# Kernel optimization log

Hardware: AMD Instinct MI355X
Metric: run time of the kernel (lower is better)

## Reference

```python
import jax, jax.numpy as jnp
import numpy as np

B, C, H, W, O = 8, 128, 256, 256, 128


def setup_inputs() -> dict:
    key = jax.random.key(0)
    k1, k2, k3, k4 = jax.random.split(key, 4)
    x = jax.random.normal(k1, (B, C, H, W), dtype=jnp.float32)
    theta_s = jax.random.uniform(k2, (C, 2), dtype=jnp.float32, minval=-1.0, maxval=1.0)
    w_dw = jax.random.normal(k3, (C,), dtype=jnp.float32) * 0.1   # depthwise 1x1, groups=C
    w_pw = jax.random.normal(k4, (O, C), dtype=jnp.float32) * (1.0 / np.sqrt(C))  # pointwise 1x1
    return {"x": x, "theta_s": theta_s, "w_dw": w_dw, "w_pw": w_pw}


def reference(x, theta_s, w_dw, w_pw):
    b, c, h, w = x.shape
    # zero pad by 1 (ZeroPad2d(1)); shift operates on the padded map, output is interior
    xp = jnp.pad(x, ((0, 0), (0, 0), (1, 1), (1, 1)))
    hp, wp = h + 2, w + 2
    t = -theta_s                      # (C, 2); torch code negates theta
    ft = jnp.floor(t)
    dt = t - ft                       # fractional part, (C, 2)
    ft = ft.astype(jnp.int32)
    # interior grid of the padded map: rows/cols 1..h / 1..w
    m = jnp.arange(1, h + 1)
    n = jnp.arange(1, w + 1)
    y0 = jnp.clip(m[None, :] + ft[:, 0:1], 0, hp - 1)      # (C, h)
    y1 = jnp.clip(m[None, :] + ft[:, 0:1] + 1, 0, hp - 1)  # (C, h)
    x0 = jnp.clip(n[None, :] + ft[:, 1:2], 0, wp - 1)      # (C, w)
    x1 = jnp.clip(n[None, :] + ft[:, 1:2] + 1, 0, wp - 1)  # (C, w)
    cidx = jnp.arange(c)[:, None, None]                    # (C,1,1)
    # gather four bilinear corners for all channels at once -> (B, C, h, w)
    z1 = xp[:, cidx, y0[:, :, None], x0[:, None, :]]
    z2 = xp[:, cidx, y0[:, :, None], x1[:, None, :]]
    z3 = xp[:, cidx, y1[:, :, None], x0[:, None, :]]
    z4 = xp[:, cidx, y1[:, :, None], x1[:, None, :]]
    dy = dt[:, 0][None, :, None, None]
    dx = dt[:, 1][None, :, None, None]
    s = (z1 * (1 - dy) * (1 - dx) + z2 * (1 - dy) * dx
         + z3 * dy * (1 - dx) + z4 * dy * dx)
    # depthwise 1x1 (groups=C): per-channel scale
    s = s * w_dw[None, :, None, None]
    # pointwise 1x1
    return jnp.einsum('bchw,oc->bohw', s, w_pw)
```

## Files before the change

### kernel.cpp

```cpp
#include <hip/hip_runtime.h>

#define B_ 8
#define C_ 128
#define H_ 256
#define W_ 256
#define O_ 128
#define PAD 136
#define WT 128

typedef __bf16 bf16x8 __attribute__((ext_vector_type(8)));
typedef float floatx4 __attribute__((ext_vector_type(4)));

__device__ __forceinline__ float ldpad(const float* __restrict__ xc, int y, int x) {
    bool in = (y >= 1) & (y <= H_) & (x >= 1) & (x <= W_);
    return in ? xc[(y - 1) * W_ + (x - 1)] : 0.0f;
}

__global__ __launch_bounds__(256, 2)
void activeshift_kernel(const float* __restrict__ x,
                        const float* __restrict__ theta,
                        const float* __restrict__ wdw,
                        const float* __restrict__ wpw,
                        float* __restrict__ out)
{
    __shared__ __align__(16) __bf16 w_lds[O_ * PAD];
    __shared__ __align__(16) __bf16 s_lds[WT * PAD];
    __shared__ int4 t_lds[C_];

    const int n  = blockIdx.x;
    const int wt = n & 1;
    const int h  = (n >> 1) & (H_ - 1);
    const int b  = n >> 9;
    const int w0 = wt * WT;
    const int tid = threadIdx.x;

    if (tid < C_) {
        float t0 = -theta[tid * 2 + 0];
        float t1 = -theta[tid * 2 + 1];
        float f0 = floorf(t0), f1 = floorf(t1);
        int4 v;
        v.x = (int)f0;
        v.y = (int)f1;
        v.z = __float_as_int(t0 - f0);
        v.w = __float_as_int(t1 - f1);
        t_lds[tid] = v;
    }

    {
        const float dwv = wdw[tid & (C_ - 1)];
        #pragma unroll
        for (int i = 0; i < 64; ++i) {
            int idx = tid + i * 256;
            int c = idx & (C_ - 1);
            int o = idx >> 7;
            w_lds[o * PAD + c] = (__bf16)(wpw[idx] * dwv);
        }
    }
    __syncthreads();

    const int p    = tid & (WT - 1);
    const int half = tid >> 7;
    const int m  = h + 1;
    const int nn = w0 + p + 1;
    const float* xb = x + (size_t)b * C_ * H_ * W_;

    for (int it = 0; it < 8; ++it) {
        int c0 = it * 16 + half * 8;
        union { bf16x8 v; __bf16 e[8]; } pk;
        #pragma unroll
        for (int cc = 0; cc < 8; ++cc) {
            int c = c0 + cc;
            int4 tv = t_lds[c];
            float dy = __int_as_float(tv.z);
            float dx = __int_as_float(tv.w);
            int y0 = m + tv.x, y1 = y0 + 1;
            int x0 = nn + tv.y, x1 = x0 + 1;
            y0 = min(max(y0, 0), H_ + 1); y1 = min(max(y1, 0), H_ + 1);
            x0 = min(max(x0, 0), W_ + 1); x1 = min(max(x1, 0), W_ + 1);
            const float* xc = xb + (size_t)c * (H_ * W_);
            float v00 = ldpad(xc, y0, x0);
            float v01 = ldpad(xc, y0, x1);
            float v10 = ldpad(xc, y1, x0);
            float v11 = ldpad(xc, y1, x1);
            float r0 = v00 + dx * (v01 - v00);
            float r1 = v10 + dx * (v11 - v10);
            pk.e[cc] = (__bf16)(r0 + dy * (r1 - r0));
        }
        *(bf16x8*)&s_lds[p * PAD + c0] = pk.v;
    }
    __syncthreads();

    const int wid  = tid >> 6;
    const int lane = tid & 63;
    const int wo   = (wid >> 1) * 64;
    const int wp   = (wid & 1) * 64;
    const int l15  = lane & 15;
    const int quad = lane >> 4;

    floatx4 acc[4][4];
    #pragma unroll
    for (int i = 0; i < 4; ++i)
        #pragma unroll
        for (int j = 0; j < 4; ++j)
            acc[i][j] = (floatx4){0.f, 0.f, 0.f, 0.f};

    #pragma unroll
    for (int k = 0; k < C_; k += 32) {
        bf16x8 af[4], bfr[4];
        #pragma unroll
        for (int i = 0; i < 4; ++i)
            af[i] = *(const bf16x8*)&w_lds[(wo + i * 16 + l15) * PAD + k + quad * 8];
        #pragma unroll
        for (int j = 0; j < 4; ++j)
            bfr[j] = *(const bf16x8*)&s_lds[(wp + j * 16 + l15) * PAD + k + quad * 8];
        #pragma unroll
        for (int i = 0; i < 4; ++i)
            #pragma unroll
            for (int j = 0; j < 4; ++j)
                acc[i][j] = __builtin_amdgcn_mfma_f32_16x16x32_bf16(af[i], bfr[j], acc[i][j], 0, 0, 0);
    }

    const size_t HW = (size_t)H_ * W_;
    float* ob = out + (size_t)b * O_ * HW + (size_t)h * W_;
    #pragma unroll
    for (int i = 0; i < 4; ++i) {
        #pragma unroll
        for (int j = 0; j < 4; ++j) {
            int pcol  = w0 + wp + j * 16 + l15;
            int obase = wo + i * 16 + quad * 4;
            float* op = ob + (size_t)obase * HW + pcol;
            #pragma unroll
            for (int r = 0; r < 4; ++r)
                op[(size_t)r * HW] = acc[i][j][r];
        }
    }
}

extern "C" void kernel_launch(void* const* d_in, const int* in_sizes, int n_in,
                              void* d_out, int out_size, void* d_ws, size_t ws_size,
                              hipStream_t stream) {
    const float* x     = (const float*)d_in[0];
    const float* theta = (const float*)d_in[1];
    const float* wdw   = (const float*)d_in[2];
    const float* wpw   = (const float*)d_in[3];
    float* out = (float*)d_out;
    dim3 grid(B_ * H_ * (W_ / WT));
    activeshift_kernel<<<grid, dim3(256), 0, stream>>>(x, theta, wdw, wpw, out);
}
```

Baseline: 535.1 us.

## Precompute per-channel bilinear weights and row offsets, scalarize, swizzle block order

Per-block setup now folds row-boundary masking into four bilinear corner weights and precomputes clamped row offsets per channel. The gather loop reads these as wave-uniform scalars via readfirstlane, which cuts per-element index math and boundary checks. Pointwise weights are loaded and converted with float4 vector accesses. Block IDs are remapped so that concurrently running blocks cover different batches, which changes which x rows and output regions are resident in cache together. The corner blend is now a direct four-term weighted sum instead of nested lerps, so rounding differs slightly.

```diff
diff --git a/kernel.cpp b/kernel.cpp
--- a/kernel.cpp
+++ b/kernel.cpp
@@ -8,12 +8,12 @@
 #define PAD 136
 #define WT 128
 
+typedef __bf16 bf16x4 __attribute__((ext_vector_type(4)));
 typedef __bf16 bf16x8 __attribute__((ext_vector_type(8)));
 typedef float floatx4 __attribute__((ext_vector_type(4)));
 
-__device__ __forceinline__ float ldpad(const float* __restrict__ xc, int y, int x) {
-    bool in = (y >= 1) & (y <= H_) & (x >= 1) & (x <= W_);
-    return in ? xc[(y - 1) * W_ + (x - 1)] : 0.0f;
+__device__ __forceinline__ float sfloat(float v) {
+    return __int_as_float(__builtin_amdgcn_readfirstlane(__float_as_int(v)));
 }
 
 __global__ __launch_bounds__(256, 2)
@@ -25,66 +25,79 @@
 {
     __shared__ __align__(16) __bf16 w_lds[O_ * PAD];
     __shared__ __align__(16) __bf16 s_lds[WT * PAD];
-    __shared__ int4 t_lds[C_];
+    __shared__ __align__(16) float  t_q[C_ * 4];
+    __shared__ __align__(16) int    t_o[C_ * 4];
 
-    const int n  = blockIdx.x;
-    const int wt = n & 1;
-    const int h  = (n >> 1) & (H_ - 1);
-    const int b  = n >> 9;
-    const int w0 = wt * WT;
+    const int bid = blockIdx.x;
+    const int n   = ((bid & 7) << 9) | (bid >> 3);
+    const int wt  = n & 1;
+    const int h   = (n >> 1) & (H_ - 1);
+    const int b   = n >> 9;
+    const int w0  = wt * WT;
     const int tid = threadIdx.x;
+    const int m   = h + 1;
 
     if (tid < C_) {
         float t0 = -theta[tid * 2 + 0];
         float t1 = -theta[tid * 2 + 1];
         float f0 = floorf(t0), f1 = floorf(t1);
-        int4 v;
-        v.x = (int)f0;
-        v.y = (int)f1;
-        v.z = __float_as_int(t0 - f0);
-        v.w = __float_as_int(t1 - f1);
-        t_lds[tid] = v;
+        float dy = t0 - f0,    dx = t1 - f1;
+        int ft0 = (int)f0, ft1 = (int)f1;
+        int y0 = m + ft0, y1 = y0 + 1;
+        float wy0 = (y0 >= 1 && y0 <= H_) ? 1.0f - dy : 0.0f;
+        float wy1 = (y1 >= 1 && y1 <= H_) ? dy : 0.0f;
+        int y0c = min(max(y0, 1), H_) - 1;
+        int y1c = min(max(y1, 1), H_) - 1;
+        *(floatx4*)&t_q[tid * 4] = (floatx4){wy0 * (1.0f - dx), wy0 * dx,
+                                             wy1 * (1.0f - dx), wy1 * dx};
+        *(int4*)&t_o[tid * 4]    = (int4){y0c * W_, y1c * W_, w0 + ft1, 0};
     }
 
     {
-        const float dwv = wdw[tid & (C_ - 1)];
+        const int c4 = (tid & 31) << 2;
+        const floatx4 dv = *(const floatx4*)&wdw[c4];
         #pragma unroll
-        for (int i = 0; i < 64; ++i) {
-            int idx = tid + i * 256;
-            int c = idx & (C_ - 1);
-            int o = idx >> 7;
-            w_lds[o * PAD + c] = (__bf16)(wpw[idx] * dwv);
+        for (int i = 0; i < 16; ++i) {
+            int idx4 = tid + i * 256;
+            int o    = idx4 >> 5;
+            floatx4 v = *(const floatx4*)&wpw[idx4 << 2];
+            bf16x4 pk = { (__bf16)(v.x * dv.x), (__bf16)(v.y * dv.y),
+                          (__bf16)(v.z * dv.z), (__bf16)(v.w * dv.w) };
+            *(bf16x4*)&w_lds[o * PAD + c4] = pk;
         }
     }
     __syncthreads();
 
-    const int p    = tid & (WT - 1);
-    const int half = tid >> 7;
-    const int m  = h + 1;
-    const int nn = w0 + p + 1;
-    const float* xb = x + (size_t)b * C_ * H_ * W_;
+    const int p     = tid & (WT - 1);
+    const int halfs = __builtin_amdgcn_readfirstlane(tid >> 7);
+    const size_t HW = (size_t)H_ * W_;
+    const float* xb = x + (size_t)b * C_ * HW;
 
     for (int it = 0; it < 8; ++it) {
-        int c0 = it * 16 + half * 8;
+        const int c0 = it * 16 + halfs * 8;
         union { bf16x8 v; __bf16 e[8]; } pk;
         #pragma unroll
         for (int cc = 0; cc < 8; ++cc) {
-            int c = c0 + cc;
-            int4 tv = t_lds[c];
-            float dy = __int_as_float(tv.z);
-            float dx = __int_as_float(tv.w);
-            int y0 = m + tv.x, y1 = y0 + 1;
-            int x0 = nn + tv.y, x1 = x0 + 1;
-            y0 = min(max(y0, 0), H_ + 1); y1 = min(max(y1, 0), H_ + 1);
-            x0 = min(max(x0, 0), W_ + 1); x1 = min(max(x1, 0), W_ + 1);
-            const float* xc = xb + (size_t)c * (H_ * W_);
-            float v00 = ldpad(xc, y0, x0);
-            float v01 = ldpad(xc, y0, x1);
-            float v10 = ldpad(xc, y1, x0);
-            float v11 = ldpad(xc, y1, x1);
-            float r0 = v00 + dx * (v01 - v00);
-            float r1 = v10 + dx * (v11 - v10);
-            pk.e[cc] = (__bf16)(r0 + dy * (r1 - r0));
+            const int c = c0 + cc;
+            const floatx4 q = *(const floatx4*)&t_q[c * 4];
+            const int4   ov = *(const int4*)&t_o[c * 4];
+            const float q00 = sfloat(q.x), q01 = sfloat(q.y);
+            const float q10 = sfloat(q.z), q11 = sfloat(q.w);
+            const int y0off = __builtin_amdgcn_readfirstlane(ov.x);
+            const int y1off = __builtin_amdgcn_readfirstlane(ov.y);
+            const int xoff  = __builtin_amdgcn_readfirstlane(ov.z);
+            const float* r0 = xb + (size_t)c * HW + y0off;
+            const float* r1 = xb + (size_t)c * HW + y1off;
+
+            const int ix0 = p + xoff;
+            const int vo0 = min(max(ix0, 0), W_ - 1);
+            const int vo1 = min(max(ix0 + 1, 0), W_ - 1);
+            float v00 = r0[vo0], v01 = r0[vo1];
+            float v10 = r1[vo0], v11 = r1[vo1];
+            if ((unsigned)ix0       > (unsigned)(W_ - 1)) { v00 = 0.f; v10 = 0.f; }
+            if ((unsigned)(ix0 + 1) > (unsigned)(W_ - 1)) { v01 = 0.f; v11 = 0.f; }
+
+            pk.e[cc] = (__bf16)(q00 * v00 + q01 * v01 + q10 * v10 + q11 * v11);
         }
         *(bf16x8*)&s_lds[p * PAD + c0] = pk.v;
     }
@@ -120,7 +133,6 @@
                 acc[i][j] = __builtin_amdgcn_mfma_f32_16x16x32_bf16(af[i], bfr[j], acc[i][j], 0, 0, 0);
     }
 
-    const size_t HW = (size_t)H_ * W_;
     float* ob = out + (size_t)b * O_ * HW + (size_t)h * W_;
     #pragma unroll
     for (int i = 0; i < 4; ++i) {
@@ -144,6 +156,5 @@
     const float* wdw   = (const float*)d_in[2];
     const float* wpw   = (const float*)d_in[3];
     float* out = (float*)d_out;
-    dim3 grid(B_ * H_ * (W_ / WT));
-    activeshift_kernel<<<grid, dim3(256), 0, stream>>>(x, theta, wdw, wpw, out);
+    activeshift_kernel<<<dim3(B_ * H_ * (W_ / WT)), dim3(256), 0, stream>>>(x, theta, wdw, wpw, out);
 }
```

Result: faster. 516.2 us (-3.5%).
